# Kernel tuning notes

Measured on AMD Instinct MI355X. Metric: run time of the kernel, lower is better.

## Reference

```python
import jax, jax.numpy as jnp
import numpy as np

B, S, H, N = 2, 2048, 1024, 16
HN = H // N  # head dim = 64
EPS = 1e-12


def setup_inputs() -> dict:
    key = jax.random.key(0)
    ks = jax.random.split(key, 8)
    scale = 0.02
    return {
        "hidden_states": jax.random.normal(ks[0], (B, S, H), dtype=jnp.float32),
        "attention_mask": jnp.zeros((B, 1, 1, S), dtype=jnp.float32),
        "W_qkv": jax.random.normal(ks[1], (3 * H, H), dtype=jnp.float32) * scale,
        "b_qkv": jnp.zeros((3 * H,), dtype=jnp.float32),
        "W_out": jax.random.normal(ks[2], (H, H), dtype=jnp.float32) * scale,
        "b_out": jnp.zeros((H,), dtype=jnp.float32),
        "ln_gamma": jnp.ones((H,), dtype=jnp.float32),
        "ln_beta": jnp.zeros((H,), dtype=jnp.float32),
    }


def reference(hidden_states, attention_mask, W_qkv, b_qkv, W_out, b_out, ln_gamma, ln_beta):
    # QKV projection: torch Linear => x @ W.T + b
    qkv = jnp.einsum("bsh,oh->bso", hidden_states, W_qkv) + b_qkv  # [B,S,3H]
    q, k, v = jnp.split(qkv, 3, axis=-1)

    def heads(t):  # [B,S,H] -> [B,N,S,HN]
        return t.reshape(B, S, N, HN).transpose(0, 2, 1, 3)

    q, k, v = heads(q), heads(k), heads(v)
    nf = jnp.sqrt(jnp.sqrt(jnp.float32(HN)))
    scores = jnp.einsum("bnsd,bntd->bnst", q / nf, k / nf) + attention_mask  # [B,N,S,S]
    probs = jax.nn.softmax(scores, axis=-1)
    ctx = jnp.einsum("bnst,bntd->bnsd", probs, v)  # [B,N,S,HN]
    ctx = ctx.transpose(0, 2, 1, 3).reshape(B, S, H)

    # output dense + residual + LayerNorm
    out = jnp.einsum("bsh,oh->bso", ctx, W_out) + b_out
    x = out + hidden_states
    mean = jnp.mean(x, axis=-1, keepdims=True)
    var = jnp.mean(jnp.square(x - mean), axis=-1, keepdims=True)
    return (x - mean) * jax.lax.rsqrt(var + EPS) * ln_gamma + ln_beta
```

## Files before the change

kernel.cpp:

```cpp
#include <hip/hip_runtime.h>
#include <hip/hip_bf16.h>
#include <math.h>

#define Bq  2
#define Sq  2048
#define Hq  1024
#define Nq  16
#define HNq 64
#define Mq  (Bq*Sq)
#define H3q (3*Hq)

#define LOG2E 1.44269504088896340736f

typedef __attribute__((ext_vector_type(8))) short           short8;
typedef __attribute__((ext_vector_type(4))) short           short4s;
typedef __attribute__((ext_vector_type(8))) unsigned short  ushortx8;
typedef __attribute__((ext_vector_type(4))) unsigned short  ushortx4;
typedef __attribute__((ext_vector_type(4))) float           floatx4;

__device__ __forceinline__ unsigned short f2bf(float f) {
    union { float f; unsigned int u; } x; x.f = f;
    unsigned int r = (x.u + 0x7fffu + ((x.u >> 16) & 1u)) >> 16;
    return (unsigned short)r;
}

__device__ __forceinline__ unsigned int pkbf(float a, float b) {
    float2 t; t.x = a; t.y = b;
    __hip_bfloat162 h = __float22bfloat162_rn(t);
    union { __hip_bfloat162 h; unsigned int u; } c; c.h = h;
    return c.u;
}

__device__ __forceinline__ float bf2f(unsigned short v) {
    union { unsigned int u; float f; } x; x.u = (unsigned int)v << 16;
    return x.f;
}

__device__ __forceinline__ float fexp2(float x) {
    float r;
    asm("v_exp_f32 %0, %1" : "=v"(r) : "v"(x));
    return r;
}

__device__ __forceinline__ void gload16(const unsigned short* g, unsigned short* l) {
    __builtin_amdgcn_global_load_lds(
        (__attribute__((address_space(1))) void*)(unsigned long long)(g),
        (__attribute__((address_space(3))) void*)(unsigned int)(unsigned long long)(l),
        16, 0, 0);
}

__device__ __forceinline__ int swz(int r) { return (r ^ (r >> 2)) & 3; }

#define N_HID ((size_t)Mq * Hq)
#define N_HW  (N_HID + (size_t)H3q * Hq)
#define N_ALL (N_HW + (size_t)Hq * Hq)
#define CVT_BLKS ((int)(N_ALL / 2048))

__global__ __launch_bounds__(256) void cvt_all(
    const float* __restrict__ hidden, const float* __restrict__ wqkv,
    const float* __restrict__ wout, const float* __restrict__ mask,
    unsigned short* __restrict__ dst, unsigned short* __restrict__ em2)
{
    const int bid = blockIdx.x;
    if (bid >= CVT_BLKS) {
        const int t0   = ((bid - CVT_BLKS) * 256 + threadIdx.x) * 8;
        const int b    = t0 >> 11;
        const int t2   = t0 & 2047;
        const int kt   = t2 >> 6;
        const int t3   = t2 & 63;
        const int ks   = t3 >> 5;
        const int quad = (t3 >> 3) & 3;
        const int kb   = kt * 64 + ks * 32 + quad * 4;
        const float* mp = mask + (size_t)b * Sq + kb;
        float4 m0 = *(const float4*)(mp);
        float4 m1 = *(const float4*)(mp + 16);
        union { unsigned int u[4]; ushortx8 s; } o;
        o.u[0] = pkbf(fexp2(m0.x * LOG2E), fexp2(m0.y * LOG2E));
        o.u[1] = pkbf(fexp2(m0.z * LOG2E), fexp2(m0.w * LOG2E));
        o.u[2] = pkbf(fexp2(m1.x * LOG2E), fexp2(m1.y * LOG2E));
        o.u[3] = pkbf(fexp2(m1.z * LOG2E), fexp2(m1.w * LOG2E));
        *(ushortx8*)(em2 + t0) = o.s;
        return;
    }
    size_t i = ((size_t)bid * 256 + threadIdx.x) * 8;
    const float* src;
    if (i < N_HID)      src = hidden + i;
    else if (i < N_HW)  src = wqkv + (i - N_HID);
    else                src = wout + (i - N_HW);
    float4 a = *(const float4*)(src);
    float4 b = *(const float4*)(src + 4);
    union { unsigned int u[4]; ushortx8 s; } o;
    o.u[0] = pkbf(a.x, a.y); o.u[1] = pkbf(a.z, a.w);
    o.u[2] = pkbf(b.x, b.y); o.u[3] = pkbf(b.z, b.w);
    *(ushortx8*)(dst + i) = o.s;
}

#define TM 128
#define TN 128
#define TK 32
#define G1M 256

__global__ __launch_bounds__(512) void gemm_mfma_qkv(
    const unsigned short* __restrict__ A, const unsigned short* __restrict__ Bw,
    const float* __restrict__ bias, const float* __restrict__ mask,
    unsigned short* __restrict__ Qb, unsigned short* __restrict__ Kd,
    unsigned short* __restrict__ V5, int K)
{
    __shared__ unsigned short As[3][G1M][TK];
    __shared__ unsigned short Bs[3][TN][TK];

    const int tid = threadIdx.x;
    const int w = tid >> 6, lane = tid & 63;
    const int l15 = lane & 15, quad = lane >> 4;
    const int wr = (w & 3) * 64;
    const int wc = (w >> 2) * 64;
    const int row0 = blockIdx.y * G1M;
    const int col0 = blockIdx.x * TN;

    const int srow16 = lane >> 2;
    const int sgd    = lane & 3;
    const int sgsrc  = (sgd ^ swz(srow16)) * 8;

    floatx4 acc[4][4];
    #pragma unroll
    for (int i = 0; i < 4; i++)
        #pragma unroll
        for (int j = 0; j < 4; j++) acc[i][j] = (floatx4){0.f,0.f,0.f,0.f};

    const int aswz = swz(l15) * 8;
    const int NK = K / TK;

    #pragma unroll
    for (int t = 0; t < 2; t++) {
        #pragma unroll
        for (int c = 0; c < 2; c++) {
            int seg = w * 2 + c;
            int r = seg * 16 + srow16;
            gload16(A + (size_t)(row0 + r) * K + t * TK + sgsrc, &As[t][seg * 16][0]);
        }
        int rB = w * 16 + srow16;
        gload16(Bw + (size_t)(col0 + rB) * K + t * TK + sgsrc, &Bs[t][w * 16][0]);
    }

    #pragma unroll 1
    for (int k = 0; k < NK; ++k) {
        if (k + 1 < NK) asm volatile("s_waitcnt vmcnt(3)" ::: "memory");
        else            asm volatile("s_waitcnt vmcnt(0)" ::: "memory");
        __builtin_amdgcn_s_barrier();
        __builtin_amdgcn_sched_barrier(0);

        const int cur = k % 3;
        if (k + 2 < NK) {
            const int nb  = (k + 2) % 3;
            const int k0n = (k + 2) * TK;
            #pragma unroll
            for (int c = 0; c < 2; c++) {
                int seg = w * 2 + c;
                int r = seg * 16 + srow16;
                gload16(A + (size_t)(row0 + r) * K + k0n + sgsrc, &As[nb][seg * 16][0]);
            }
            int rB = w * 16 + srow16;
            gload16(Bw + (size_t)(col0 + rB) * K + k0n + sgsrc, &Bs[nb][w * 16][0]);
        }
        __builtin_amdgcn_sched_barrier(0);

        short8 af[4], bf[4];
        #pragma unroll
        for (int i = 0; i < 4; i++)
            af[i] = *(const short8*)&As[cur][wr + i * 16 + l15][(quad * 8) ^ aswz];
        #pragma unroll
        for (int j = 0; j < 4; j++)
            bf[j] = *(const short8*)&Bs[cur][wc + j * 16 + l15][(quad * 8) ^ aswz];
        __builtin_amdgcn_s_setprio(1);
        #pragma unroll
        for (int i = 0; i < 4; i++)
            #pragma unroll
            for (int j = 0; j < 4; j++)
                acc[i][j] = __builtin_amdgcn_mfma_f32_16x16x32_bf16(af[i], bf[j], acc[i][j], 0, 0, 0);
        __builtin_amdgcn_s_setprio(0);
    }

    const int cls = col0 >> 10;

    if (cls == 2) {
        #pragma unroll
        for (int i = 0; i < 4; i++) {
            const int rb = row0 + wr + i * 16 + quad * 4;
            const int b  = rb >> 11;
            const int s  = rb & (Sq - 1);
            const int kt32 = s >> 6;
            const int sw   = s & 63;
            const int kg   = sw >> 2;
            const int ks   = kg >> 3;
            const int q2   = kg & 3;
            const int hi   = (kg >> 2) & 1;
            float expm[4];
            #pragma unroll
            for (int rr = 0; rr < 4; rr++)
                expm[rr] = fexp2(mask[(size_t)b * Sq + s + rr] * LOG2E);
            #pragma unroll
            for (int j = 0; j < 4; j++) {
                const int c  = col0 + wc + j * 16 + l15;
                const int c2 = c - 2 * Hq;
                const int n  = c2 >> 6, d = c2 & 63;
                const int dt = d >> 4, dl = d & 15;
                const float bia = bias[c];
                ushortx4 o;
                #pragma unroll
                for (int rr = 0; rr < 4; rr++)
                    o[rr] = f2bf((acc[i][j][rr] + bia) * expm[rr]);
                const size_t off = (((size_t)(b * Nq + n) * 32 + kt32) << 12)
                                 + (size_t)((ks * 16 + dt * 4 + q2) * 128 + dl * 8 + hi * 4);
                *(ushortx4*)&V5[off] = o;
            }
        }
    } else {
        unsigned short* __restrict__ dst = (cls == 0) ? Qb : Kd;
        const int cshift = (cls == 0) ? 0 : Hq;
        const float qs = (cls == 0) ? (0.125f * LOG2E) : 1.0f;
        #pragma unroll
        for (int i = 0; i < 4; i++) {
            const int rb = row0 + wr + i * 16 + quad * 4;
            #pragma unroll
            for (int j = 0; j < 4; j++) {
                const int c = col0 + wc + j * 16 + l15;
                const float bia = bias[c];
                #pragma unroll
                for (int rr = 0; rr < 4; rr++)
                    dst[(size_t)(rb + rr) * Hq + (c - cshift)] =
                        f2bf((acc[i][j][rr] + bia) * qs);
            }
        }
    }
}

#define T2M 64
#define T2N 128

__global__ __launch_bounds__(256) void gemm_mfma_out(
    const unsigned short* __restrict__ A, const unsigned short* __restrict__ Bw,
    const float* __restrict__ bias, const float* __restrict__ res,
    unsigned short* __restrict__ X, int M, int Nd, int K)
{
    __shared__ unsigned short As[3][T2M][TK];
    __shared__ unsigned short Bs[3][T2N][TK];

    const int tid = threadIdx.x;
    const int w = tid >> 6, lane = tid & 63;
    const int l15 = lane & 15, quad = lane >> 4;
    const int wr = (w & 1) * 32;
    const int wc = (w >> 1) * 64;
    const int row0 = blockIdx.y * T2M;
    const int col0 = blockIdx.x * T2N;

    const int srow16 = lane >> 2;
    const int sgd    = lane & 3;
    const int sgsrc  = (sgd ^ swz(srow16)) * 8;

    floatx4 acc[2][4];
    #pragma unroll
    for (int i = 0; i < 2; i++)
        #pragma unroll
        for (int j = 0; j < 4; j++) acc[i][j] = (floatx4){0.f,0.f,0.f,0.f};

    const int aswz = swz(l15) * 8;
    const int NK = K / TK;

    #pragma unroll
    for (int t = 0; t < 2; t++) {
        int rA = w * 16 + srow16;
        gload16(A + (size_t)(row0 + rA) * K + t * TK + sgsrc, &As[t][w * 16][0]);
        #pragma unroll
        for (int c = 0; c < 2; c++) {
            int seg = w * 2 + c;
            int rB = seg * 16 + srow16;
            gload16(Bw + (size_t)(col0 + rB) * K + t * TK + sgsrc, &Bs[t][seg * 16][0]);
        }
    }

    #pragma unroll 1
    for (int k = 0; k < NK; ++k) {
        if (k + 1 < NK) asm volatile("s_waitcnt vmcnt(3)" ::: "memory");
        else            asm volatile("s_waitcnt vmcnt(0)" ::: "memory");
        __builtin_amdgcn_s_barrier();
        __builtin_amdgcn_sched_barrier(0);

        const int cur = k % 3;
        if (k + 2 < NK) {
            const int nb  = (k + 2) % 3;
            const int k0n = (k + 2) * TK;
            int rA = w * 16 + srow16;
            gload16(A + (size_t)(row0 + rA) * K + k0n + sgsrc, &As[nb][w * 16][0]);
            #pragma unroll
            for (int c = 0; c < 2; c++) {
                int seg = w * 2 + c;
                int rB = seg * 16 + srow16;
                gload16(Bw + (size_t)(col0 + rB) * K + k0n + sgsrc, &Bs[nb][seg * 16][0]);
            }
        }
        __builtin_amdgcn_sched_barrier(0);

        short8 af[2], bf[4];
        #pragma unroll
        for (int i = 0; i < 2; i++)
            af[i] = *(const short8*)&As[cur][wr + i * 16 + l15][(quad * 8) ^ aswz];
        #pragma unroll
        for (int j = 0; j < 4; j++)
            bf[j] = *(const short8*)&Bs[cur][wc + j * 16 + l15][(quad * 8) ^ aswz];
        __builtin_amdgcn_s_setprio(1);
        #pragma unroll
        for (int i = 0; i < 2; i++)
            #pragma unroll
            for (int j = 0; j < 4; j++)
                acc[i][j] = __builtin_amdgcn_mfma_f32_16x16x32_bf16(af[i], bf[j], acc[i][j], 0, 0, 0);
        __builtin_amdgcn_s_setprio(0);
    }

    #pragma unroll
    for (int i = 0; i < 2; i++) {
        const int rb = row0 + wr + i * 16 + quad * 4;
        #pragma unroll
        for (int j = 0; j < 4; j++) {
            const int c = col0 + wc + j * 16 + l15;
            const float bia = bias[c];
            #pragma unroll
            for (int rr = 0; rr < 4; rr++) {
                X[(size_t)(rb + rr) * Nd + c] =
                    f2bf(acc[i][j][rr] + bia + res[(size_t)(rb + rr) * Nd + c]);
            }
        }
    }
}

#define KTILES 16

__device__ __forceinline__ floatx4 mfma16(short8 a, short8 b, floatx4 c) {
    return __builtin_amdgcn_mfma_f32_16x16x32_bf16(a, b, c, 0, 0, 0);
}

__device__ __forceinline__ void do_lpv(
    const short8 (&pf0)[2], const short8 (&pf1)[2], const short8 (&mf)[2],
    const unsigned short* Vt,
    floatx4 (&oacc0)[4], floatx4 (&oacc1)[4],
    floatx4 &lacc0, floatx4 &lacc1)
{
    __builtin_amdgcn_s_setprio(1);
    lacc0 = mfma16(mf[0], pf0[0], lacc0);
    lacc0 = mfma16(mf[1], pf0[1], lacc0);
    lacc1 = mfma16(mf[0], pf1[0], lacc1);
    lacc1 = mfma16(mf[1], pf1[1], lacc1);
    #pragma unroll
    for (int dt = 0; dt < 4; dt++) {
        short8 vlo = *(const short8*)(Vt + dt * 512);
        short8 vhi = *(const short8*)(Vt + 2048 + dt * 512);
        oacc0[dt] = mfma16(vlo, pf0[0], oacc0[dt]);
        oacc1[dt] = mfma16(vlo, pf1[0], oacc1[dt]);
        oacc0[dt] = mfma16(vhi, pf0[1], oacc0[dt]);
        oacc1[dt] = mfma16(vhi, pf1[1], oacc1[dt]);
    }
    __builtin_amdgcn_s_setprio(0);
}

template<bool HAVER, bool PREF>
__device__ __forceinline__ void attn_body(
    int kt,
    unsigned short (&KsL)[2][64][64],
    unsigned short (&VsL)[3][4096],
    const unsigned short* kp, size_t kstep,
    const unsigned short* Vb, const unsigned short* e2b,
    int w, int l15, int quad, int lane,
    const short8 (&qf0)[2], const short8 (&qf1)[2],
    const short8 (&pfR0)[2], const short8 (&pfR1)[2], const short8 (&mfR)[2],
    short8 (&pfW0)[2], short8 (&pfW1)[2], short8 (&mfW)[2],
    floatx4 (&oacc0)[4], floatx4 (&oacc1)[4],
    floatx4 &lacc0, floatx4 &lacc1)
{
    asm volatile("s_waitcnt vmcnt(0)" ::: "memory");
    __builtin_amdgcn_s_barrier();
    __builtin_amdgcn_sched_barrier(0);

    if (PREF) {
        const unsigned short* kpn = kp + (size_t)(kt + 1) * kstep;
        gload16(kpn,                  &KsL[(kt + 1) & 1][w * 16][0]);
        gload16(kpn + (size_t)8 * Hq, &KsL[(kt + 1) & 1][w * 16 + 8][0]);
        const unsigned short* vpn = Vb + (size_t)(kt + 1) * 4096 + w * 1024 + lane * 8;
        unsigned short* vd = &VsL[(kt + 1) % 3][w * 1024];
        gload16(vpn,       vd);
        gload16(vpn + 512, vd + 512);
    }
    __builtin_amdgcn_sched_barrier(0);

    const unsigned short* ep = e2b + kt * 64;
    mfW[0] = *(const short8*)(ep + quad * 8);
    mfW[1] = *(const short8*)(ep + 32 + quad * 8);

    floatx4 s0[4], s1[4];
    #pragma unroll
    for (int ct = 0; ct < 4; ct++) {
        s0[ct] = (floatx4){0.f,0.f,0.f,0.f};
        s1[ct] = (floatx4){0.f,0.f,0.f,0.f};
    }
    __builtin_amdgcn_s_setprio(1);
    #pragma unroll
    for (int ks = 0; ks < 2; ks++) {
        #pragma unroll
        for (int ct = 0; ct < 4; ct++) {
            short8 af = *(const short8*)&KsL[kt & 1][ct * 16 + l15][((4 * ks + quad) ^ (l15 & 7)) * 8];
            s0[ct] = mfma16(af, qf0[ks], s0[ct]);
            s1[ct] = mfma16(af, qf1[ks], s1[ct]);
        }
    }
    __builtin_amdgcn_s_setprio(0);

    #pragma unroll
    for (int ks = 0; ks < 2; ks++) {
        union { unsigned int u[4]; short8 s; } pk;
        #pragma unroll
        for (int h = 0; h < 2; h++) {
            const int ct = ks * 2 + h;
            pk.u[h * 2]     = pkbf(fexp2(s0[ct][0]), fexp2(s0[ct][1]));
            pk.u[h * 2 + 1] = pkbf(fexp2(s0[ct][2]), fexp2(s0[ct][3]));
        }
        pfW0[ks] = pk.s;
    }
    #pragma unroll
    for (int ks = 0; ks < 2; ks++) {
        union { unsigned int u[4]; short8 s; } pk;
        #pragma unroll
        for (int h = 0; h < 2; h++) {
            const int ct = ks * 2 + h;
            pk.u[h * 2]     = pkbf(fexp2(s1[ct][0]), fexp2(s1[ct][1]));
            pk.u[h * 2 + 1] = pkbf(fexp2(s1[ct][2]), fexp2(s1[ct][3]));
        }
        pfW1[ks] = pk.s;
    }

    if (HAVER)
        do_lpv(pfR0, pfR1, mfR, &VsL[(kt - 1) % 3][0] + lane * 8,
               oacc0, oacc1, lacc0, lacc1);
}

__global__ __launch_bounds__(256) void attn_mfma(
    const unsigned short* __restrict__ Qb, const unsigned short* __restrict__ Kd,
    const unsigned short* __restrict__ V5, const unsigned short* __restrict__ em2,
    unsigned short* __restrict__ Opart, float* __restrict__ Lpart)
{
    __shared__ unsigned short Ks[2][64][64];
    __shared__ unsigned short Vs[3][4096];

    const int tid  = threadIdx.x;
    const int w    = tid >> 6;
    const int lane = tid & 63;
    const int l15  = lane & 15;
    const int quad = lane >> 4;

    const int i_    = blockIdx.x;
    const int gl8   = i_ & 7;
    const int rest  = i_ >> 3;
    const int qtile = rest & 15;
    const int g     = (rest >> 4) * 8 + gl8;
    const int bn    = g >> 1;
    const int z     = g & 1;
    const int n     = bn & 15;
    const int b     = bn >> 4;

    const int kbase = z * (KTILES * 64);

    short8 qf0[2], qf1[2];
    {
        const int qrow0 = qtile * 128 + w * 16 + l15;
        const unsigned short* qp = Qb + (size_t)(b * Sq + qrow0) * Hq + n * HNq + quad * 8;
        qf0[0] = *(const short8*)(qp);
        qf0[1] = *(const short8*)(qp + 32);
        qp += (size_t)64 * Hq;
        qf1[0] = *(const short8*)(qp);
        qf1[1] = *(const short8*)(qp + 32);
    }

    floatx4 oacc0[4], oacc1[4];
    #pragma unroll
    for (int dt = 0; dt < 4; dt++) {
        oacc0[dt] = (floatx4){0.f,0.f,0.f,0.f};
        oacc1[dt] = (floatx4){0.f,0.f,0.f,0.f};
    }
    floatx4 lacc0 = (floatx4){0.f,0.f,0.f,0.f};
    floatx4 lacc1 = (floatx4){0.f,0.f,0.f,0.f};

    const int krow8 = lane >> 3;
    const int kgr   = (lane & 7) ^ (krow8 & 7);
    const unsigned short* kp = Kd + (size_t)(b * Sq + kbase + w * 16 + krow8) * Hq
                                  + n * HNq + kgr * 8;
    const size_t kstep = (size_t)64 * Hq;

    const unsigned short* Vb  = V5 + ((size_t)(b * Nq + n) * 32 + z * KTILES) * 4096;
    const unsigned short* e2b = em2 + (size_t)(b * 32 + z * KTILES) * 64;

    gload16(kp,                  &Ks[0][w * 16][0]);
    gload16(kp + (size_t)8 * Hq, &Ks[0][w * 16 + 8][0]);
    {
        const unsigned short* vp0 = Vb + w * 1024 + lane * 8;
        gload16(vp0,       &Vs[0][w * 1024]);
        gload16(vp0 + 512, &Vs[0][w * 1024] + 512);
    }

    short8 pfA0[2], pfA1[2], mfA[2];
    short8 pfB0[2], pfB1[2], mfB[2];

    attn_body<false, true>(0, Ks, Vs, kp, kstep, Vb, e2b, w, l15, quad, lane,
        qf0, qf1, pfB0, pfB1, mfB, pfA0, pfA1, mfA, oacc0, oacc1, lacc0, lacc1);

    #pragma unroll 1
    for (int kt = 1; kt < KTILES - 1; kt += 2) {
        attn_body<true, true>(kt, Ks, Vs, kp, kstep, Vb, e2b, w, l15, quad, lane,
            qf0, qf1, pfA0, pfA1, mfA, pfB0, pfB1, mfB, oacc0, oacc1, lacc0, lacc1);
        attn_body<true, true>(kt + 1, Ks, Vs, kp, kstep, Vb, e2b, w, l15, quad, lane,
            qf0, qf1, pfB0, pfB1, mfB, pfA0, pfA1, mfA, oacc0, oacc1, lacc0, lacc1);
    }
    attn_body<true, false>(KTILES - 1, Ks, Vs, kp, kstep, Vb, e2b, w, l15, quad, lane,
        qf0, qf1, pfA0, pfA1, mfA, pfB0, pfB1, mfB, oacc0, oacc1, lacc0, lacc1);
    do_lpv(pfB0, pfB1, mfB, &Vs[(KTILES - 1) % 3][0] + lane * 8,
           oacc0, oacc1, lacc0, lacc1);

    unsigned short* Ow = Opart + (size_t)z * Mq * Hq;
    #pragma unroll
    for (int sub = 0; sub < 2; sub++) {
        const float l_i = sub ? lacc1[0] : lacc0[0];
        const int qrow = qtile * 128 + sub * 64 + w * 16 + l15;
        if (quad == 0)
            Lpart[(size_t)z * Mq * Nq + (size_t)(b * Sq + qrow) * Nq + n] = l_i;
        #pragma unroll
        for (int dt = 0; dt < 4; dt++) {
            const floatx4 oa = sub ? oacc1[dt] : oacc0[dt];
            union { unsigned int u[2]; ushortx4 s; } o;
            o.u[0] = pkbf(oa[0], oa[1]);
            o.u[1] = pkbf(oa[2], oa[3]);
            const int col = n * HNq + dt * 16 + quad * 4;
            *(ushortx4*)&Ow[(size_t)(b * Sq + qrow) * Hq + col] = o.s;
        }
    }
}

__global__ __launch_bounds__(256) void attn_merge(
    const unsigned short* __restrict__ Opart, const float* __restrict__ Lpart,
    unsigned short* __restrict__ ctx)
{
    const size_t idx = ((size_t)blockIdx.x * 256 + threadIdx.x) * 4;
    const int row = (int)(idx >> 10);
    const int n   = ((int)idx >> 6) & 15;
    const float l = Lpart[(size_t)row * Nq + n]
                  + Lpart[(size_t)Mq * Nq + (size_t)row * Nq + n];
    const float inv = 1.0f / l;
    ushortx4 a = *(const ushortx4*)(Opart + idx);
    ushortx4 c = *(const ushortx4*)(Opart + (size_t)Mq * Hq + idx);
    union { unsigned int u[2]; ushortx4 s; } o;
    o.u[0] = pkbf((bf2f(a[0]) + bf2f(c[0])) * inv, (bf2f(a[1]) + bf2f(c[1])) * inv);
    o.u[1] = pkbf((bf2f(a[2]) + bf2f(c[2])) * inv, (bf2f(a[3]) + bf2f(c[3])) * inv);
    *(ushortx4*)(ctx + idx) = o.s;
}

__global__ __launch_bounds__(256) void ln_kernel(
    const unsigned short* __restrict__ X, const float* __restrict__ gamma,
    const float* __restrict__ beta, float* __restrict__ out)
{
    const int row = blockIdx.x;
    const int c0  = threadIdx.x * 4;
    ushortx4 xv = *(const ushortx4*)(X + (size_t)row * Hq + c0);
    float vals[4];
    float lsum = 0.0f;
    #pragma unroll
    for (int i = 0; i < 4; i++) { vals[i] = bf2f(xv[i]); lsum += vals[i]; }

    __shared__ float red[8];
    const int wid = threadIdx.x >> 6, lane = threadIdx.x & 63;

    float s = lsum;
    #pragma unroll
    for (int off = 32; off >= 1; off >>= 1) s += __shfl_xor(s, off, 64);
    if (lane == 0) red[wid] = s;
    __syncthreads();
    const float mean = (red[0] + red[1] + red[2] + red[3]) * (1.0f / Hq);

    float v = 0.0f;
    #pragma unroll
    for (int i = 0; i < 4; i++) { float d = vals[i] - mean; v += d * d; }
    #pragma unroll
    for (int off = 32; off >= 1; off >>= 1) v += __shfl_xor(v, off, 64);
    if (lane == 0) red[4 + wid] = v;
    __syncthreads();
    const float var  = (red[4] + red[5] + red[6] + red[7]) * (1.0f / Hq);
    const float rstd = rsqrtf(var + 1e-12f);

    float4 gm = *(const float4*)(gamma + c0);
    float4 bt = *(const float4*)(beta + c0);
    float4 o;
    o.x = (vals[0] - mean) * rstd * gm.x + bt.x;
    o.y = (vals[1] - mean) * rstd * gm.y + bt.y;
    o.z = (vals[2] - mean) * rstd * gm.z + bt.z;
    o.w = (vals[3] - mean) * rstd * gm.w + bt.w;
    *(float4*)(out + (size_t)row * Hq + c0) = o;
}

extern "C" void kernel_launch(void* const* d_in, const int* in_sizes, int n_in,
                              void* d_out, int out_size, void* d_ws, size_t ws_size,
                              hipStream_t stream)
{
    const float* hidden = (const float*)d_in[0];
    const float* mask   = (const float*)d_in[1];
    const float* W_qkv  = (const float*)d_in[2];
    const float* b_qkv  = (const float*)d_in[3];
    const float* W_out  = (const float*)d_in[4];
    const float* b_out  = (const float*)d_in[5];
    const float* gamma  = (const float*)d_in[6];
    const float* beta   = (const float*)d_in[7];
    float* out = (float*)d_out;

    const size_t nHid  = (size_t)Mq * Hq;
    const size_t nWq   = (size_t)H3q * Hq;
    const size_t nWo   = (size_t)Hq * Hq;
    const size_t nCtx  = (size_t)Mq * Hq;

    unsigned short* hidden_bf = (unsigned short*)d_ws;
    unsigned short* Wqkv_bf   = hidden_bf + nHid;
    unsigned short* Wout_bf   = Wqkv_bf + nWq;
    unsigned short* qb        = Wout_bf + nWo;
    unsigned short* kd        = qb + nHid;
    unsigned short* v5        = kd + nHid;
    unsigned short* ctx_bf    = v5 + nHid;
    unsigned short* x_bf      = ctx_bf + nCtx;
    unsigned short* opart     = x_bf + nHid;
    float*          lpart     = (float*)(opart + 2 * nHid);
    unsigned short* em2       = (unsigned short*)(lpart + 2 * (size_t)Mq * Nq);

    dim3 blk(256);

    cvt_all<<<dim3(CVT_BLKS + 2), blk, 0, stream>>>(
        hidden, W_qkv, W_out, mask, hidden_bf, em2);

    gemm_mfma_qkv<<<dim3(H3q / TN, Mq / G1M), dim3(512), 0, stream>>>(
        hidden_bf, Wqkv_bf, b_qkv, mask, qb, kd, v5, Hq);

    attn_mfma<<<dim3(1024), blk, 0, stream>>>(
        qb, kd, v5, em2, opart, lpart);

    attn_merge<<<dim3((int)(nCtx / 1024)), blk, 0, stream>>>(
        opart, lpart, ctx_bf);

    gemm_mfma_out<<<dim3(Hq / T2N, Mq / T2M), blk, 0, stream>>>(
        ctx_bf, Wout_bf, b_out, hidden, x_bf, Mq, Hq, Hq);

    ln_kernel<<<dim3(Mq), blk, 0, stream>>>(x_bf, gamma, beta, out);
}
```

Baseline: 199.9 us.

## Drop attention KV split, interleave swizzled K and V tiles, remove merge kernel

The attention kernel no longer splits each head's key range in two. Each block now walks all 32 key tiles and normalises its output in place, so the partial-output buffers and the separate merge kernel go away. The QKV GEMM epilogue writes K into a pre-swizzled tiled layout interleaved with V, so each key tile's K and V sit next to each other and load as one contiguous stream. In exchange the attention launch has half as many blocks, which may reduce occupancy and parallelism on the GPU, and the K epilogue now does scattered 2-byte stores.

```diff
diff --git a/kernel.cpp b/kernel.cpp
--- a/kernel.cpp
+++ b/kernel.cpp
@@ -103,8 +103,7 @@
 __global__ __launch_bounds__(512) void gemm_mfma_qkv(
     const unsigned short* __restrict__ A, const unsigned short* __restrict__ Bw,
     const float* __restrict__ bias, const float* __restrict__ mask,
-    unsigned short* __restrict__ Qb, unsigned short* __restrict__ Kd,
-    unsigned short* __restrict__ V5, int K)
+    unsigned short* __restrict__ Qb, unsigned short* __restrict__ KV5, int K)
 {
     __shared__ unsigned short As[3][G1M][TK];
     __shared__ unsigned short Bs[3][TN][TK];
@@ -209,15 +208,36 @@
                 #pragma unroll
                 for (int rr = 0; rr < 4; rr++)
                     o[rr] = f2bf((acc[i][j][rr] + bia) * expm[rr]);
-                const size_t off = (((size_t)(b * Nq + n) * 32 + kt32) << 12)
+                const size_t off = (((size_t)(b * Nq + n) * 32 + kt32) << 13) + 4096
                                  + (size_t)((ks * 16 + dt * 4 + q2) * 128 + dl * 8 + hi * 4);
-                *(ushortx4*)&V5[off] = o;
+                *(ushortx4*)&KV5[off] = o;
             }
         }
+    } else if (cls == 1) {
+        #pragma unroll
+        for (int i = 0; i < 4; i++) {
+            const int rb = row0 + wr + i * 16 + quad * 4;
+            #pragma unroll
+            for (int j = 0; j < 4; j++) {
+                const int c  = col0 + wc + j * 16 + l15;
+                const int c2 = c - Hq;
+                const int n  = c2 >> 6, d = c2 & 63;
+                const float bia = bias[c];
+                #pragma unroll
+                for (int rr = 0; rr < 4; rr++) {
+                    const int srow = rb + rr;
+                    const int b    = srow >> 11;
+                    const int s    = srow & (Sq - 1);
+                    const int kt32 = s >> 6;
+                    const int r    = s & 63;
+                    const size_t off = (((size_t)(b * Nq + n) * 32 + kt32) << 13)
+                                     + (size_t)(r * 64 + (((d >> 3) ^ (r & 7)) * 8 + (d & 7)));
+                    KV5[off] = f2bf(acc[i][j][rr] + bia);
+                }
+            }
+        }
     } else {
-        unsigned short* __restrict__ dst = (cls == 0) ? Qb : Kd;
-        const int cshift = (cls == 0) ? 0 : Hq;
-        const float qs = (cls == 0) ? (0.125f * LOG2E) : 1.0f;
+        const float qs = 0.125f * LOG2E;
         #pragma unroll
         for (int i = 0; i < 4; i++) {
             const int rb = row0 + wr + i * 16 + quad * 4;
@@ -227,7 +247,7 @@
                 const float bia = bias[c];
                 #pragma unroll
                 for (int rr = 0; rr < 4; rr++)
-                    dst[(size_t)(rb + rr) * Hq + (c - cshift)] =
+                    Qb[(size_t)(rb + rr) * Hq + c] =
                         f2bf((acc[i][j][rr] + bia) * qs);
             }
         }
@@ -332,7 +352,7 @@
     }
 }
 
-#define KTILES 16
+#define KTILES 32
 
 __device__ __forceinline__ floatx4 mfma16(short8 a, short8 b, floatx4 c) {
     return __builtin_amdgcn_mfma_f32_16x16x32_bf16(a, b, c, 0, 0, 0);
@@ -366,8 +386,7 @@
     int kt,
     unsigned short (&KsL)[2][64][64],
     unsigned short (&VsL)[3][4096],
-    const unsigned short* kp, size_t kstep,
-    const unsigned short* Vb, const unsigned short* e2b,
+    const unsigned short* KVb, const unsigned short* e2b,
     int w, int l15, int quad, int lane,
     const short8 (&qf0)[2], const short8 (&qf1)[2],
     const short8 (&pfR0)[2], const short8 (&pfR1)[2], const short8 (&mfR)[2],
@@ -380,13 +399,12 @@
     __builtin_amdgcn_sched_barrier(0);
 
     if (PREF) {
-        const unsigned short* kpn = kp + (size_t)(kt + 1) * kstep;
-        gload16(kpn,                  &KsL[(kt + 1) & 1][w * 16][0]);
-        gload16(kpn + (size_t)8 * Hq, &KsL[(kt + 1) & 1][w * 16 + 8][0]);
-        const unsigned short* vpn = Vb + (size_t)(kt + 1) * 4096 + w * 1024 + lane * 8;
+        const unsigned short* tb = KVb + (size_t)(kt + 1) * 8192 + w * 1024 + lane * 8;
+        gload16(tb,        &KsL[(kt + 1) & 1][w * 16][0]);
+        gload16(tb + 512,  &KsL[(kt + 1) & 1][w * 16 + 8][0]);
         unsigned short* vd = &VsL[(kt + 1) % 3][w * 1024];
-        gload16(vpn,       vd);
-        gload16(vpn + 512, vd + 512);
+        gload16(tb + 4096,       vd);
+        gload16(tb + 4096 + 512, vd + 512);
     }
     __builtin_amdgcn_sched_barrier(0);
 
@@ -441,9 +459,8 @@
 }
 
 __global__ __launch_bounds__(256) void attn_mfma(
-    const unsigned short* __restrict__ Qb, const unsigned short* __restrict__ Kd,
-    const unsigned short* __restrict__ V5, const unsigned short* __restrict__ em2,
-    unsigned short* __restrict__ Opart, float* __restrict__ Lpart)
+    const unsigned short* __restrict__ Qb, const unsigned short* __restrict__ KV5,
+    const unsigned short* __restrict__ em2, unsigned short* __restrict__ ctx)
 {
     __shared__ unsigned short Ks[2][64][64];
     __shared__ unsigned short Vs[3][4096];
@@ -459,12 +476,8 @@
     const int rest  = i_ >> 3;
     const int qtile = rest & 15;
     const int g     = (rest >> 4) * 8 + gl8;
-    const int bn    = g >> 1;
-    const int z     = g & 1;
-    const int n     = bn & 15;
-    const int b     = bn >> 4;
-
-    const int kbase = z * (KTILES * 64);
+    const int n     = g & 15;
+    const int b     = g >> 4;
 
     short8 qf0[2], qf1[2];
     {
@@ -486,76 +499,49 @@
     floatx4 lacc0 = (floatx4){0.f,0.f,0.f,0.f};
     floatx4 lacc1 = (floatx4){0.f,0.f,0.f,0.f};
 
-    const int krow8 = lane >> 3;
-    const int kgr   = (lane & 7) ^ (krow8 & 7);
-    const unsigned short* kp = Kd + (size_t)(b * Sq + kbase + w * 16 + krow8) * Hq
-                                  + n * HNq + kgr * 8;
-    const size_t kstep = (size_t)64 * Hq;
-
-    const unsigned short* Vb  = V5 + ((size_t)(b * Nq + n) * 32 + z * KTILES) * 4096;
-    const unsigned short* e2b = em2 + (size_t)(b * 32 + z * KTILES) * 64;
-
-    gload16(kp,                  &Ks[0][w * 16][0]);
-    gload16(kp + (size_t)8 * Hq, &Ks[0][w * 16 + 8][0]);
+    const unsigned short* KVb = KV5 + (size_t)(b * Nq + n) * 32 * 8192;
+    const unsigned short* e2b = em2 + (size_t)b * 32 * 64;
+
     {
-        const unsigned short* vp0 = Vb + w * 1024 + lane * 8;
-        gload16(vp0,       &Vs[0][w * 1024]);
-        gload16(vp0 + 512, &Vs[0][w * 1024] + 512);
+        const unsigned short* tb = KVb + w * 1024 + lane * 8;
+        gload16(tb,        &Ks[0][w * 16][0]);
+        gload16(tb + 512,  &Ks[0][w * 16 + 8][0]);
+        gload16(tb + 4096,       &Vs[0][w * 1024]);
+        gload16(tb + 4096 + 512, &Vs[0][w * 1024] + 512);
     }
 
     short8 pfA0[2], pfA1[2], mfA[2];
     short8 pfB0[2], pfB1[2], mfB[2];
 
-    attn_body<false, true>(0, Ks, Vs, kp, kstep, Vb, e2b, w, l15, quad, lane,
+    attn_body<false, true>(0, Ks, Vs, KVb, e2b, w, l15, quad, lane,
         qf0, qf1, pfB0, pfB1, mfB, pfA0, pfA1, mfA, oacc0, oacc1, lacc0, lacc1);
 
     #pragma unroll 1
     for (int kt = 1; kt < KTILES - 1; kt += 2) {
-        attn_body<true, true>(kt, Ks, Vs, kp, kstep, Vb, e2b, w, l15, quad, lane,
+        attn_body<true, true>(kt, Ks, Vs, KVb, e2b, w, l15, quad, lane,
             qf0, qf1, pfA0, pfA1, mfA, pfB0, pfB1, mfB, oacc0, oacc1, lacc0, lacc1);
-        attn_body<true, true>(kt + 1, Ks, Vs, kp, kstep, Vb, e2b, w, l15, quad, lane,
+        attn_body<true, true>(kt + 1, Ks, Vs, KVb, e2b, w, l15, quad, lane,
             qf0, qf1, pfB0, pfB1, mfB, pfA0, pfA1, mfA, oacc0, oacc1, lacc0, lacc1);
     }
-    attn_body<true, false>(KTILES - 1, Ks, Vs, kp, kstep, Vb, e2b, w, l15, quad, lane,
+    attn_body<true, false>(KTILES - 1, Ks, Vs, KVb, e2b, w, l15, quad, lane,
         qf0, qf1, pfA0, pfA1, mfA, pfB0, pfB1, mfB, oacc0, oacc1, lacc0, lacc1);
     do_lpv(pfB0, pfB1, mfB, &Vs[(KTILES - 1) % 3][0] + lane * 8,
            oacc0, oacc1, lacc0, lacc1);
 
-    unsigned short* Ow = Opart + (size_t)z * Mq * Hq;
     #pragma unroll
     for (int sub = 0; sub < 2; sub++) {
-        const float l_i = sub ? lacc1[0] : lacc0[0];
+        const float inv = 1.0f / (sub ? lacc1[0] : lacc0[0]);
         const int qrow = qtile * 128 + sub * 64 + w * 16 + l15;
-        if (quad == 0)
-            Lpart[(size_t)z * Mq * Nq + (size_t)(b * Sq + qrow) * Nq + n] = l_i;
         #pragma unroll
         for (int dt = 0; dt < 4; dt++) {
             const floatx4 oa = sub ? oacc1[dt] : oacc0[dt];
             union { unsigned int u[2]; ushortx4 s; } o;
-            o.u[0] = pkbf(oa[0], oa[1]);
-            o.u[1] = pkbf(oa[2], oa[3]);
+            o.u[0] = pkbf(oa[0] * inv, oa[1] * inv);
+            o.u[1] = pkbf(oa[2] * inv, oa[3] * inv);
             const int col = n * HNq + dt * 16 + quad * 4;
-            *(ushortx4*)&Ow[(size_t)(b * Sq + qrow) * Hq + col] = o.s;
-        }
-    }
-}
-
-__global__ __launch_bounds__(256) void attn_merge(
-    const unsigned short* __restrict__ Opart, const float* __restrict__ Lpart,
-    unsigned short* __restrict__ ctx)
-{
-    const size_t idx = ((size_t)blockIdx.x * 256 + threadIdx.x) * 4;
-    const int row = (int)(idx >> 10);
-    const int n   = ((int)idx >> 6) & 15;
-    const float l = Lpart[(size_t)row * Nq + n]
-                  + Lpart[(size_t)Mq * Nq + (size_t)row * Nq + n];
-    const float inv = 1.0f / l;
-    ushortx4 a = *(const ushortx4*)(Opart + idx);
-    ushortx4 c = *(const ushortx4*)(Opart + (size_t)Mq * Hq + idx);
-    union { unsigned int u[2]; ushortx4 s; } o;
-    o.u[0] = pkbf((bf2f(a[0]) + bf2f(c[0])) * inv, (bf2f(a[1]) + bf2f(c[1])) * inv);
-    o.u[1] = pkbf((bf2f(a[2]) + bf2f(c[2])) * inv, (bf2f(a[3]) + bf2f(c[3])) * inv);
-    *(ushortx4*)(ctx + idx) = o.s;
+            *(ushortx4*)&ctx[(size_t)(b * Sq + qrow) * Hq + col] = o.s;
+        }
+    }
 }
 
 __global__ __launch_bounds__(256) void ln_kernel(
@@ -617,19 +603,15 @@
     const size_t nHid  = (size_t)Mq * Hq;
     const size_t nWq   = (size_t)H3q * Hq;
     const size_t nWo   = (size_t)Hq * Hq;
-    const size_t nCtx  = (size_t)Mq * Hq;
 
     unsigned short* hidden_bf = (unsigned short*)d_ws;
     unsigned short* Wqkv_bf   = hidden_bf + nHid;
     unsigned short* Wout_bf   = Wqkv_bf + nWq;
     unsigned short* qb        = Wout_bf + nWo;
-    unsigned short* kd        = qb + nHid;
-    unsigned short* v5        = kd + nHid;
-    unsigned short* ctx_bf    = v5 + nHid;
-    unsigned short* x_bf      = ctx_bf + nCtx;
-    unsigned short* opart     = x_bf + nHid;
-    float*          lpart     = (float*)(opart + 2 * nHid);
-    unsigned short* em2       = (unsigned short*)(lpart + 2 * (size_t)Mq * Nq);
+    unsigned short* kv5       = qb + nHid;
+    unsigned short* ctx_bf    = kv5 + 2 * nHid;
+    unsigned short* x_bf      = ctx_bf + nHid;
+    unsigned short* em2       = x_bf + nHid;
 
     dim3 blk(256);
 
@@ -637,13 +619,10 @@
         hidden, W_qkv, W_out, mask, hidden_bf, em2);
 
     gemm_mfma_qkv<<<dim3(H3q / TN, Mq / G1M), dim3(512), 0, stream>>>(
-        hidden_bf, Wqkv_bf, b_qkv, mask, qb, kd, v5, Hq);
-
-    attn_mfma<<<dim3(1024), blk, 0, stream>>>(
-        qb, kd, v5, em2, opart, lpart);
-
-    attn_merge<<<dim3((int)(nCtx / 1024)), blk, 0, stream>>>(
-        opart, lpart, ctx_bf);
+        hidden_bf, Wqkv_bf, b_qkv, mask, qb, kv5, Hq);
+
+    attn_mfma<<<dim3(512), blk, 0, stream>>>(
+        qb, kv5, em2, ctx_bf);
 
     gemm_mfma_out<<<dim3(Hq / T2N, Mq / T2M), blk, 0, stream>>>(
         ctx_bf, Wout_bf, b_out, hidden, x_bf, Mq, Hq, Hq);
```

Result: faster. 193.7 us (-3.1%).
